# Optimization experiments

Hardware: AMD Instinct MI355X
Metric: run time of the kernel (lower is better)

The kernel has to match this reference:

```python
import jax, jax.numpy as jnp
import numpy as np

SIZE = 512
NUM_HEADS = 8
HEAD_SIZE = SIZE // NUM_HEADS
EPS = 1e-5  # GroupNorm default eps


def setup_inputs() -> dict:
    key = jax.random.key(0)
    ks = jax.random.split(key, 8)
    B, T, D = 2, 2048, SIZE
    mk = lambda k: jax.random.normal(k, (D, D), dtype=jnp.float32) / D
    return {
        "x": jax.random.normal(ks[0], (B, T, D), dtype=jnp.float32),
        "W_Q": mk(ks[1]),
        "W_K": mk(ks[2]),
        "W_V": mk(ks[3]),
        "W_G": mk(ks[4]),
        "W_O": mk(ks[5]),
        "gn_weight": jnp.ones((D,), dtype=jnp.float32),
        "gn_bias": jnp.zeros((D,), dtype=jnp.float32),
    }


def _retention(x, W_Q, W_K, W_V):
    B, T, D = x.shape
    H, dh = NUM_HEADS, HEAD_SIZE
    # projections -> (B, H, T, dh)
    q = (x @ W_Q).reshape(B, T, H, dh).transpose(0, 2, 1, 3)
    k = (x @ W_K).reshape(B, T, H, dh).transpose(0, 2, 1, 3)
    v = (x @ W_V).reshape(B, T, H, dh).transpose(0, 2, 1, 3)
    # multi-scale per-head decay: gamma_h = 1 - 2^{-5-h}
    gammas = 1.0 - jnp.exp2(-5.0 - jnp.arange(H, dtype=jnp.float32))
    idx = jnp.arange(T)
    diff = (idx[:, None] - idx[None, :]).astype(jnp.float32)  # (T, T)
    causal = diff >= 0
    # D[h, n, m] = gamma_h^{n-m} for n >= m else 0
    decay = jnp.where(causal[None], jnp.exp(diff[None] * jnp.log(gammas)[:, None, None]), 0.0)
    scores = jnp.einsum("bhtd,bhsd->bhts", q, k) / jnp.sqrt(jnp.float32(dh))
    out = jnp.einsum("bhts,bhsd->bhtd", scores * decay[None], v)
    return out.transpose(0, 2, 1, 3).reshape(B, T, D)


def _group_norm(y, weight, bias):
    # GroupNorm(NUM_HEADS, SIZE) over flattened (B*T, SIZE)
    B, T, D = y.shape
    g = y.reshape(B * T, NUM_HEADS, HEAD_SIZE)
    mean = jnp.mean(g, axis=-1, keepdims=True)
    var = jnp.var(g, axis=-1, keepdims=True)
    g = (g - mean) / jnp.sqrt(var + EPS)
    g = g.reshape(B * T, D) * weight + bias
    return g.reshape(B, T, D)


def reference(x, W_Q, W_K, W_V, W_G, W_O, gn_weight, gn_bias):
    ret = _retention(x, W_Q, W_K, W_V)          # (B, T, D)
    normed = _group_norm(ret, gn_weight, gn_bias)  # (B, T, D)
    return jax.nn.silu(x @ W_G + normed) @ W_O
```

## Files before the change

### kernel.cpp

```cpp
#include <hip/hip_runtime.h>
#include <hip/hip_bf16.h>
#include <math.h>

#define DMODEL 512
#define T_SEQ 2048
#define NH 8
#define DH 64
#define M_ROWS 4096
#define LDST 72

typedef short s16x8 __attribute__((ext_vector_type(8)));
typedef float f32x4 __attribute__((ext_vector_type(4)));

static __device__ __forceinline__ unsigned short f2bf(float f) {
  __hip_bfloat16 h = __float2bfloat16(f);
  return *(unsigned short*)&h;
}
static __device__ __forceinline__ float bf2f(unsigned short u) {
  union { unsigned int i; float f; } x; x.i = (unsigned int)u << 16; return x.f;
}
static __device__ __forceinline__ void gld16(void* lds, const void* g) {
  __builtin_amdgcn_global_load_lds(
      (const __attribute__((address_space(1))) unsigned int*)g,
      (__attribute__((address_space(3))) unsigned int*)lds, 16, 0, 0);
}

__global__ __launch_bounds__(256) void prep_k(
    const float* __restrict__ x, unsigned short* __restrict__ Xb,
    const float* __restrict__ W0, const float* __restrict__ W1,
    const float* __restrict__ W2, const float* __restrict__ W3,
    const float* __restrict__ W4, unsigned short* __restrict__ WT)
{
  __shared__ __align__(16) unsigned short buf[64 * LDST];
  const int bid = blockIdx.x, tid = threadIdx.x;
  if (bid < 1024) {
    const size_t i = ((size_t)bid * 256 + tid) * 8;
    float4 a = *(const float4*)&x[i];
    float4 b = *(const float4*)&x[i + 4];
    s16x8 o;
    o[0]=f2bf(a.x); o[1]=f2bf(a.y); o[2]=f2bf(a.z); o[3]=f2bf(a.w);
    o[4]=f2bf(b.x); o[5]=f2bf(b.y); o[6]=f2bf(b.z); o[7]=f2bf(b.w);
    *(s16x8*)&Xb[i] = o;
    return;
  }
  const int bid2 = bid - 1024;
  const int z = bid2 >> 6, rem = bid2 & 63;
  const int n0 = (rem & 7) * 64, k0 = (rem >> 3) * 64;
  const float* W = (z==0)?W0:(z==1)?W1:(z==2)?W2:(z==3)?W3:W4;
  #pragma unroll
  for (int r = 0; r < 4; ++r) {
    int idx = r * 256 + tid;
    int kr = idx >> 4, nc = idx & 15;
    float4 v = *(const float4*)&W[(size_t)(k0 + kr) * DMODEL + n0 + nc * 4];
    buf[(nc*4+0) * LDST + kr] = f2bf(v.x);
    buf[(nc*4+1) * LDST + kr] = f2bf(v.y);
    buf[(nc*4+2) * LDST + kr] = f2bf(v.z);
    buf[(nc*4+3) * LDST + kr] = f2bf(v.w);
  }
  __syncthreads();
  #pragma unroll
  for (int r = 0; r < 2; ++r) {
    int idx = r * 256 + tid;
    int nr = idx >> 3, c = idx & 7;
    *(s16x8*)&WT[((size_t)z * DMODEL + n0 + nr) * DMODEL + k0 + c * 8] =
        *(const s16x8*)&buf[nr * LDST + c * 8];
  }
}

__global__ __launch_bounds__(256) void mfma_gemm_k(
    const unsigned short* __restrict__ A, const unsigned short* __restrict__ BT,
    unsigned short* __restrict__ C0, unsigned short* __restrict__ C1,
    unsigned short* __restrict__ C2, unsigned short* __restrict__ C3)
{
  __shared__ __align__(16) unsigned short As[128 * 64];
  __shared__ __align__(16) unsigned short Bs[128 * 64];
  const int ng0 = blockIdx.x * 128;
  const int m0 = blockIdx.y * 128;
  const int z = ng0 >> 9, n0 = ng0 & 511;
  unsigned short* Cz = (z==0)?C0:(z==1)?C1:(z==2)?C2:C3;
  const int tid = threadIdx.x;
  const int wave = tid >> 6, lane = tid & 63;
  const int wm = wave >> 1, wn = wave & 1;
  const int n = lane & 15, quad = lane >> 4;

  int srow[4], scol[4];
  #pragma unroll
  for (int r = 0; r < 4; ++r) {
    int idx = r * 256 + tid;
    srow[r] = idx >> 3;
    scol[r] = ((idx & 7) ^ (srow[r] & 7)) * 8;
  }

  f32x4 acc[4][4];
  #pragma unroll
  for (int mi = 0; mi < 4; ++mi)
    #pragma unroll
    for (int ni = 0; ni < 4; ++ni) acc[mi][ni] = (f32x4){0.f,0.f,0.f,0.f};

  for (int k0 = 0; k0 < 512; k0 += 64) {
    #pragma unroll
    for (int r = 0; r < 4; ++r) {
      int idx = r * 256 + tid;
      gld16(&As[idx * 8], &A[(size_t)(m0 + srow[r]) * DMODEL + k0 + scol[r]]);
      gld16(&Bs[idx * 8], &BT[(size_t)(ng0 + srow[r]) * DMODEL + k0 + scol[r]]);
    }
    __syncthreads();
    #pragma unroll
    for (int kk = 0; kk < 2; ++kk) {
      s16x8 af[4], bf[4];
      #pragma unroll
      for (int mi = 0; mi < 4; ++mi) {
        int R = wm*64 + mi*16 + n, cc = (kk*4 + quad) ^ (n & 7);
        af[mi] = *(const s16x8*)&As[R * 64 + cc * 8];
      }
      #pragma unroll
      for (int ni = 0; ni < 4; ++ni) {
        int R = wn*64 + ni*16 + n, cc = (kk*4 + quad) ^ (n & 7);
        bf[ni] = *(const s16x8*)&Bs[R * 64 + cc * 8];
      }
      #pragma unroll
      for (int mi = 0; mi < 4; ++mi)
        #pragma unroll
        for (int ni = 0; ni < 4; ++ni)
          acc[mi][ni] = __builtin_amdgcn_mfma_f32_16x16x32_bf16(
              af[mi], bf[ni], acc[mi][ni], 0, 0, 0);
    }
    __syncthreads();
  }

  #pragma unroll
  for (int mi = 0; mi < 4; ++mi)
    #pragma unroll
    for (int ni = 0; ni < 4; ++ni)
      #pragma unroll
      for (int r = 0; r < 4; ++r)
        Cz[(size_t)(m0 + wm*64 + mi*16 + quad*4 + r) * DMODEL +
           n0 + wn*64 + ni*16 + n] = f2bf(acc[mi][ni][r]);
}

__global__ __launch_bounds__(256) void ret_kv_k(
    const unsigned short* __restrict__ Kb, const unsigned short* __restrict__ Vb,
    float* __restrict__ AT)
{
  __shared__ __align__(16) unsigned short Kts[64 * LDST];
  __shared__ __align__(16) unsigned short Vts[64 * LDST];
  const int c = blockIdx.x, h = blockIdx.y, b = blockIdx.z;
  const int bh = b * NH + h;
  const int tid = threadIdx.x;
  const int wave = tid >> 6, lane = tid & 63;
  const int n = lane & 15, quad = lane >> 4;
  const size_t base = ((size_t)b * T_SEQ + (size_t)c * 64) * DMODEL + h * DH;
  const float lg = log2f(1.0f - exp2f(-5.0f - (float)h));

  #pragma unroll
  for (int r = 0; r < 2; ++r) {
    int idx = r * 256 + tid;
    int m = idx & 63, ch = idx >> 6;
    s16x8 kv = *(const s16x8*)&Kb[base + (size_t)m * DMODEL + ch * 8];
    s16x8 vv = *(const s16x8*)&Vb[base + (size_t)m * DMODEL + ch * 8];
    float sc = exp2f((float)(64 - m) * lg);
    #pragma unroll
    for (int e = 0; e < 8; ++e) {
      Kts[(ch * 8 + e) * LDST + m] = f2bf(bf2f(((unsigned short*)&kv)[e]) * sc);
      Vts[(ch * 8 + e) * LDST + m] = ((unsigned short*)&vv)[e];
    }
  }
  __syncthreads();

  f32x4 at[4];
  #pragma unroll
  for (int j = 0; j < 4; ++j) at[j] = (f32x4){0.f,0.f,0.f,0.f};
  #pragma unroll
  for (int kk = 0; kk < 2; ++kk) {
    s16x8 a = *(const s16x8*)&Vts[(wave*16 + n) * LDST + kk*32 + quad*8];
    #pragma unroll
    for (int j = 0; j < 4; ++j) {
      s16x8 bf = *(const s16x8*)&Kts[(j*16 + n) * LDST + kk*32 + quad*8];
      at[j] = __builtin_amdgcn_mfma_f32_16x16x32_bf16(a, bf, at[j], 0, 0, 0);
    }
  }
  float* Ab = AT + (((size_t)bh * 32 + c) << 12);
  #pragma unroll
  for (int j = 0; j < 4; ++j)
    #pragma unroll
    for (int r = 0; r < 4; ++r)
      Ab[(wave*16 + quad*4 + r) * 64 + j*16 + n] = at[j][r];
}

__global__ __launch_bounds__(256) void ret_o2_k(
    const unsigned short* __restrict__ Qb, const unsigned short* __restrict__ Kb,
    const unsigned short* __restrict__ Vb, const float* __restrict__ AT,
    const unsigned short* __restrict__ Gg, const float* __restrict__ gnw,
    const float* __restrict__ gnb, unsigned short* __restrict__ Sb)
{
  __shared__ __align__(16) unsigned short Qs[64 * LDST];
  __shared__ __align__(16) unsigned short Ks[64 * LDST];
  __shared__ __align__(16) unsigned short Vst[64 * LDST];
  __shared__ __align__(16) unsigned short Ss[64 * LDST];
  __shared__ __align__(16) unsigned short Ps[64 * LDST];
  const int c = (int)gridDim.x - 1 - (int)blockIdx.x;
  const int h = blockIdx.y, b = blockIdx.z;
  const int bh = b * NH + h;
  const int tid = threadIdx.x;
  const int wave = tid >> 6, lane = tid & 63;
  const int n = lane & 15, quad = lane >> 4;
  const size_t base = ((size_t)b * T_SEQ + (size_t)c * 64) * DMODEL + h * DH;
  const float lg = log2f(1.0f - exp2f(-5.0f - (float)h));
  const float g64 = exp2f(64.0f * lg);

  #pragma unroll
  for (int r = 0; r < 2; ++r) {
    int idx = r * 256 + tid;
    int i = idx >> 3, ch = idx & 7;
    *(s16x8*)&Qs[i * LDST + ch * 8] =
        *(const s16x8*)&Qb[base + (size_t)i * DMODEL + ch * 8];
    *(s16x8*)&Ks[i * LDST + ch * 8] =
        *(const s16x8*)&Kb[base + (size_t)i * DMODEL + ch * 8];
  }
  #pragma unroll
  for (int r = 0; r < 2; ++r) {
    int idx = r * 256 + tid;
    int m = idx & 63, ch = idx >> 6;
    s16x8 vv = *(const s16x8*)&Vb[base + (size_t)m * DMODEL + ch * 8];
    #pragma unroll
    for (int e = 0; e < 8; ++e)
      Vst[(ch * 8 + e) * LDST + m] = ((unsigned short*)&vv)[e];
  }

  const float* Ac = AT + (((size_t)bh * 32) << 12) + (size_t)tid * 16;
  float4 S0 = {0,0,0,0}, S1 = S0, S2 = S0, S3 = S0;
  if (c > 0) {
    float4 n0 = *(const float4*)(Ac + 0);
    float4 n1 = *(const float4*)(Ac + 4);
    float4 n2 = *(const float4*)(Ac + 8);
    float4 n3 = *(const float4*)(Ac + 12);
    for (int cp = 0; cp < c; ++cp) {
      float4 a0 = n0, a1 = n1, a2 = n2, a3 = n3;
      if (cp + 1 < c) {
        const float* p = Ac + ((size_t)(cp + 1) << 12);
        n0 = *(const float4*)(p + 0);  n1 = *(const float4*)(p + 4);
        n2 = *(const float4*)(p + 8);  n3 = *(const float4*)(p + 12);
      }
      S0.x = fmaf(g64, S0.x, a0.x); S0.y = fmaf(g64, S0.y, a0.y);
      S0.z = fmaf(g64, S0.z, a0.z); S0.w = fmaf(g64, S0.w, a0.w);
      S1.x = fmaf(g64, S1.x, a1.x); S1.y = fmaf(g64, S1.y, a1.y);
      S1.z = fmaf(g64, S1.z, a1.z); S1.w = fmaf(g64, S1.w, a1.w);
      S2.x = fmaf(g64, S2.x, a2.x); S2.y = fmaf(g64, S2.y, a2.y);
      S2.z = fmaf(g64, S2.z, a2.z); S2.w = fmaf(g64, S2.w, a2.w);
      S3.x = fmaf(g64, S3.x, a3.x); S3.y = fmaf(g64, S3.y, a3.y);
      S3.z = fmaf(g64, S3.z, a3.z); S3.w = fmaf(g64, S3.w, a3.w);
    }
  }
  {
    const int d2 = tid >> 2, d1b = (tid & 3) * 16;
    s16x8 lo, hi;
    lo[0]=f2bf(S0.x); lo[1]=f2bf(S0.y); lo[2]=f2bf(S0.z); lo[3]=f2bf(S0.w);
    lo[4]=f2bf(S1.x); lo[5]=f2bf(S1.y); lo[6]=f2bf(S1.z); lo[7]=f2bf(S1.w);
    hi[0]=f2bf(S2.x); hi[1]=f2bf(S2.y); hi[2]=f2bf(S2.z); hi[3]=f2bf(S2.w);
    hi[4]=f2bf(S3.x); hi[5]=f2bf(S3.y); hi[6]=f2bf(S3.z); hi[7]=f2bf(S3.w);
    *(s16x8*)&Ss[d2 * LDST + d1b] = lo;
    *(s16x8*)&Ss[d2 * LDST + d1b + 8] = hi;
  }
  __syncthreads();

  f32x4 s[4], u[4];
  #pragma unroll
  for (int j = 0; j < 4; ++j) {
    s[j] = (f32x4){0.f,0.f,0.f,0.f};
    u[j] = (f32x4){0.f,0.f,0.f,0.f};
  }
  #pragma unroll
  for (int kk = 0; kk < 2; ++kk) {
    s16x8 a = *(const s16x8*)&Qs[(wave*16 + n) * LDST + kk*32 + quad*8];
    #pragma unroll
    for (int j = 0; j < 4; ++j) {
      s16x8 bk = *(const s16x8*)&Ks[(j*16 + n) * LDST + kk*32 + quad*8];
      s[j] = __builtin_amdgcn_mfma_f32_16x16x32_bf16(a, bk, s[j], 0, 0, 0);
      s16x8 bs = *(const s16x8*)&Ss[(j*16 + n) * LDST + kk*32 + quad*8];
      u[j] = __builtin_amdgcn_mfma_f32_16x16x32_bf16(a, bs, u[j], 0, 0, 0);
    }
  }

  float rowf[4], colf[4];
  #pragma unroll
  for (int r = 0; r < 4; ++r) rowf[r] = exp2f((float)(wave*16 + quad*4 + r) * lg);
  #pragma unroll
  for (int j = 0; j < 4; ++j) colf[j] = exp2f(-(float)(j*16 + n) * lg);

  #pragma unroll
  for (int j = 0; j < 4; ++j)
    #pragma unroll
    for (int r = 0; r < 4; ++r) {
      int i = wave*16 + quad*4 + r, mcol = j*16 + n;
      float v = (mcol <= i) ? s[j][r] * 0.125f * rowf[r] * colf[j] : 0.0f;
      Ps[i * LDST + mcol] = f2bf(v);
    }
  __syncthreads();

  f32x4 acc[4];
  #pragma unroll
  for (int j = 0; j < 4; ++j) acc[j] = (f32x4){0.f,0.f,0.f,0.f};
  #pragma unroll
  for (int kk = 0; kk < 2; ++kk) {
    s16x8 a = *(const s16x8*)&Ps[(wave*16 + n) * LDST + kk*32 + quad*8];
    #pragma unroll
    for (int j = 0; j < 4; ++j) {
      s16x8 bf = *(const s16x8*)&Vst[(j*16 + n) * LDST + kk*32 + quad*8];
      acc[j] = __builtin_amdgcn_mfma_f32_16x16x32_bf16(a, bf, acc[j], 0, 0, 0);
    }
  }

  float ov[4][4];
  #pragma unroll
  for (int j = 0; j < 4; ++j)
    #pragma unroll
    for (int r = 0; r < 4; ++r)
      ov[j][r] = acc[j][r] + 0.125f * rowf[r] * u[j][r];

  float gw[4], gb[4];
  #pragma unroll
  for (int j = 0; j < 4; ++j) {
    gw[j] = gnw[h*DH + j*16 + n];
    gb[j] = gnb[h*DH + j*16 + n];
  }

  #pragma unroll
  for (int r = 0; r < 4; ++r) {
    float sum = ov[0][r] + ov[1][r] + ov[2][r] + ov[3][r];
    float sq  = ov[0][r]*ov[0][r] + ov[1][r]*ov[1][r]
              + ov[2][r]*ov[2][r] + ov[3][r]*ov[3][r];
    #pragma unroll
    for (int off = 8; off > 0; off >>= 1) {
      sum += __shfl_xor(sum, off, 64);
      sq  += __shfl_xor(sq,  off, 64);
    }
    const float mean = sum * (1.0f / 64.0f);
    float var = sq * (1.0f / 64.0f) - mean * mean;
    var = fmaxf(var, 0.0f);
    const float rstd = rsqrtf(var + 1e-5f);
    const int i = wave*16 + quad*4 + r;
    const size_t rowoff = base + (size_t)i * DMODEL;
    #pragma unroll
    for (int j = 0; j < 4; ++j) {
      float normed = (ov[j][r] - mean) * rstd * gw[j] + gb[j];
      float uu = bf2f(Gg[rowoff + j*16 + n]) + normed;
      Sb[rowoff + j*16 + n] = f2bf(uu / (1.0f + expf(-uu)));
    }
  }
}

__global__ __launch_bounds__(256) void out_gemm_k(
    const unsigned short* __restrict__ A, const unsigned short* __restrict__ BT,
    float* __restrict__ out)
{
  __shared__ __align__(16) unsigned short As[128 * 64];
  __shared__ __align__(16) unsigned short Bs[128 * 64];
  const int n0 = blockIdx.x * 128;
  const int m0 = blockIdx.y * 128;
  const int tid = threadIdx.x;
  const int wave = tid >> 6, lane = tid & 63;
  const int wm = wave >> 1, wn = wave & 1;
  const int n = lane & 15, quad = lane >> 4;

  int srow[4], scol[4];
  #pragma unroll
  for (int r = 0; r < 4; ++r) {
    int idx = r * 256 + tid;
    srow[r] = idx >> 3;
    scol[r] = ((idx & 7) ^ (srow[r] & 7)) * 8;
  }

  f32x4 acc[4][4];
  #pragma unroll
  for (int mi = 0; mi < 4; ++mi)
    #pragma unroll
    for (int ni = 0; ni < 4; ++ni) acc[mi][ni] = (f32x4){0.f,0.f,0.f,0.f};

  for (int k0 = 0; k0 < 512; k0 += 64) {
    #pragma unroll
    for (int r = 0; r < 4; ++r) {
      int idx = r * 256 + tid;
      gld16(&As[idx * 8], &A[(size_t)(m0 + srow[r]) * DMODEL + k0 + scol[r]]);
      gld16(&Bs[idx * 8], &BT[(size_t)(n0 + srow[r]) * DMODEL + k0 + scol[r]]);
    }
    __syncthreads();
    #pragma unroll
    for (int kk = 0; kk < 2; ++kk) {
      s16x8 af[4], bf[4];
      #pragma unroll
      for (int mi = 0; mi < 4; ++mi) {
        int R = wm*64 + mi*16 + n, cc = (kk*4 + quad) ^ (n & 7);
        af[mi] = *(const s16x8*)&As[R * 64 + cc * 8];
      }
      #pragma unroll
      for (int ni = 0; ni < 4; ++ni) {
        int R = wn*64 + ni*16 + n, cc = (kk*4 + quad) ^ (n & 7);
        bf[ni] = *(const s16x8*)&Bs[R * 64 + cc * 8];
      }
      #pragma unroll
      for (int mi = 0; mi < 4; ++mi)
        #pragma unroll
        for (int ni = 0; ni < 4; ++ni)
          acc[mi][ni] = __builtin_amdgcn_mfma_f32_16x16x32_bf16(
              af[mi], bf[ni], acc[mi][ni], 0, 0, 0);
    }
    __syncthreads();
  }

  #pragma unroll
  for (int mi = 0; mi < 4; ++mi)
    #pragma unroll
    for (int ni = 0; ni < 4; ++ni)
      #pragma unroll
      for (int r = 0; r < 4; ++r)
        out[(size_t)(m0 + wm*64 + mi*16 + quad*4 + r) * DMODEL +
            n0 + wn*64 + ni*16 + n] = acc[mi][ni][r];
}

extern "C" void kernel_launch(void* const* d_in, const int* in_sizes, int n_in,
                              void* d_out, int out_size, void* d_ws, size_t ws_size,
                              hipStream_t stream) {
  const float* x   = (const float*)d_in[0];
  const float* WQ  = (const float*)d_in[1];
  const float* WK  = (const float*)d_in[2];
  const float* WV  = (const float*)d_in[3];
  const float* WG  = (const float*)d_in[4];
  const float* WO  = (const float*)d_in[5];
  const float* gnw = (const float*)d_in[6];
  const float* gnb = (const float*)d_in[7];
  float* out = (float*)d_out;

  char* ws = (char*)d_ws;
  unsigned short* Xb = (unsigned short*)(ws);
  unsigned short* Qb = (unsigned short*)(ws + 4  * (1<<20));
  unsigned short* Kb = (unsigned short*)(ws + 8  * (1<<20));
  unsigned short* Vb = (unsigned short*)(ws + 12 * (1<<20));
  unsigned short* G  = (unsigned short*)(ws + 16 * (1<<20));
  float* AT  = (float*)(ws + 24 * (1<<20));
  unsigned short* Sb = (unsigned short*)(ws + 32 * (1<<20));
  unsigned short* WT = (unsigned short*)(ws + 40 * (1<<20));
  (void)ws_size;

  prep_k<<<dim3(1024 + 320), 256, 0, stream>>>(x, Xb, WQ, WK, WV, WG, WO, WT);
  mfma_gemm_k<<<dim3(16, M_ROWS / 128), 256, 0, stream>>>(
      Xb, WT, Qb, Kb, Vb, G);
  ret_kv_k<<<dim3(T_SEQ / 64, NH, 2), 256, 0, stream>>>(Kb, Vb, AT);
  ret_o2_k<<<dim3(T_SEQ / 64, NH, 2), 256, 0, stream>>>(
      Qb, Kb, Vb, AT, G, gnw, gnb, Sb);
  out_gemm_k<<<dim3(4, M_ROWS / 128), 256, 0, stream>>>(
      Sb, WT + 4 * DMODEL * DMODEL, out);
}
```

Measured before the change: 130.0 us.

## Fuse chunk KV-state computation into projection GEMM epilogue; shrink output GEMM tile

Result: faster. 125.5 us (-3.4%).

```diff
diff --git a/kernel.cpp b/kernel.cpp
--- a/kernel.cpp
+++ b/kernel.cpp
@@ -47,6 +47,12 @@
   const int z = bid2 >> 6, rem = bid2 & 63;
   const int n0 = (rem & 7) * 64, k0 = (rem >> 3) * 64;
   const float* W = (z==0)?W0:(z==1)?W1:(z==2)?W2:(z==3)?W3:W4;
+  int rowbase;
+  if (z == 0)      rowbase = n0;
+  else if (z == 1) rowbase = 512 + (n0 >> 6) * 128;
+  else if (z == 2) rowbase = 512 + (n0 >> 6) * 128 + 64;
+  else if (z == 3) rowbase = 1536 + n0;
+  else             rowbase = 2048 + n0;
   #pragma unroll
   for (int r = 0; r < 4; ++r) {
     int idx = r * 256 + tid;
@@ -62,22 +68,22 @@
   for (int r = 0; r < 2; ++r) {
     int idx = r * 256 + tid;
     int nr = idx >> 3, c = idx & 7;
-    *(s16x8*)&WT[((size_t)z * DMODEL + n0 + nr) * DMODEL + k0 + c * 8] =
+    *(s16x8*)&WT[((size_t)(rowbase + nr)) * DMODEL + k0 + c * 8] =
         *(const s16x8*)&buf[nr * LDST + c * 8];
   }
 }
 
-__global__ __launch_bounds__(256) void mfma_gemm_k(
+__global__ __launch_bounds__(256) void proj_kv_k(
     const unsigned short* __restrict__ A, const unsigned short* __restrict__ BT,
-    unsigned short* __restrict__ C0, unsigned short* __restrict__ C1,
-    unsigned short* __restrict__ C2, unsigned short* __restrict__ C3)
+    unsigned short* __restrict__ Qb, unsigned short* __restrict__ Kb,
+    unsigned short* __restrict__ Vb, unsigned short* __restrict__ Gb,
+    float* __restrict__ AT)
 {
-  __shared__ __align__(16) unsigned short As[128 * 64];
-  __shared__ __align__(16) unsigned short Bs[128 * 64];
+  __shared__ __align__(16) unsigned short smem[2 * 128 * 64];
+  unsigned short* As = smem;
+  unsigned short* Bs = smem + 128 * 64;
   const int ng0 = blockIdx.x * 128;
   const int m0 = blockIdx.y * 128;
-  const int z = ng0 >> 9, n0 = ng0 & 511;
-  unsigned short* Cz = (z==0)?C0:(z==1)?C1:(z==2)?C2:C3;
   const int tid = threadIdx.x;
   const int wave = tid >> 6, lane = tid & 63;
   const int wm = wave >> 1, wn = wave & 1;
@@ -128,63 +134,73 @@
     __syncthreads();
   }
 
+  const int bx = blockIdx.x;
+  if (bx < 4 || bx >= 12) {
+    unsigned short* Cz = (bx < 4) ? Qb : Gb;
+    const int n0 = (bx < 4) ? ng0 : (ng0 - 1536);
+    #pragma unroll
+    for (int mi = 0; mi < 4; ++mi)
+      #pragma unroll
+      for (int ni = 0; ni < 4; ++ni)
+        #pragma unroll
+        for (int r = 0; r < 4; ++r)
+          Cz[(size_t)(m0 + wm*64 + mi*16 + quad*4 + r) * DMODEL +
+             n0 + wn*64 + ni*16 + n] = f2bf(acc[mi][ni][r]);
+    return;
+  }
+
+  const int h = (ng0 - 512) >> 7;
+  const float lg = log2f(1.0f - exp2f(-5.0f - (float)h));
+  unsigned short* KVo = (wn == 0) ? Kb : Vb;
   #pragma unroll
   for (int mi = 0; mi < 4; ++mi)
     #pragma unroll
     for (int ni = 0; ni < 4; ++ni)
       #pragma unroll
       for (int r = 0; r < 4; ++r)
-        Cz[(size_t)(m0 + wm*64 + mi*16 + quad*4 + r) * DMODEL +
-           n0 + wn*64 + ni*16 + n] = f2bf(acc[mi][ni][r]);
-}
-
-__global__ __launch_bounds__(256) void ret_kv_k(
-    const unsigned short* __restrict__ Kb, const unsigned short* __restrict__ Vb,
-    float* __restrict__ AT)
-{
-  __shared__ __align__(16) unsigned short Kts[64 * LDST];
-  __shared__ __align__(16) unsigned short Vts[64 * LDST];
-  const int c = blockIdx.x, h = blockIdx.y, b = blockIdx.z;
-  const int bh = b * NH + h;
-  const int tid = threadIdx.x;
-  const int wave = tid >> 6, lane = tid & 63;
-  const int n = lane & 15, quad = lane >> 4;
-  const size_t base = ((size_t)b * T_SEQ + (size_t)c * 64) * DMODEL + h * DH;
-  const float lg = log2f(1.0f - exp2f(-5.0f - (float)h));
-
-  #pragma unroll
-  for (int r = 0; r < 2; ++r) {
-    int idx = r * 256 + tid;
-    int m = idx & 63, ch = idx >> 6;
-    s16x8 kv = *(const s16x8*)&Kb[base + (size_t)m * DMODEL + ch * 8];
-    s16x8 vv = *(const s16x8*)&Vb[base + (size_t)m * DMODEL + ch * 8];
-    float sc = exp2f((float)(64 - m) * lg);
-    #pragma unroll
-    for (int e = 0; e < 8; ++e) {
-      Kts[(ch * 8 + e) * LDST + m] = f2bf(bf2f(((unsigned short*)&kv)[e]) * sc);
-      Vts[(ch * 8 + e) * LDST + m] = ((unsigned short*)&vv)[e];
-    }
-  }
-  __syncthreads();
-
-  f32x4 at[4];
-  #pragma unroll
-  for (int j = 0; j < 4; ++j) at[j] = (f32x4){0.f,0.f,0.f,0.f};
-  #pragma unroll
-  for (int kk = 0; kk < 2; ++kk) {
-    s16x8 a = *(const s16x8*)&Vts[(wave*16 + n) * LDST + kk*32 + quad*8];
-    #pragma unroll
-    for (int j = 0; j < 4; ++j) {
-      s16x8 bf = *(const s16x8*)&Kts[(j*16 + n) * LDST + kk*32 + quad*8];
-      at[j] = __builtin_amdgcn_mfma_f32_16x16x32_bf16(a, bf, at[j], 0, 0, 0);
-    }
-  }
-  float* Ab = AT + (((size_t)bh * 32 + c) << 12);
-  #pragma unroll
-  for (int j = 0; j < 4; ++j)
-    #pragma unroll
-    for (int r = 0; r < 4; ++r)
-      Ab[(wave*16 + quad*4 + r) * 64 + j*16 + n] = at[j][r];
+        KVo[(size_t)(m0 + wm*64 + mi*16 + quad*4 + r) * DMODEL +
+            h*DH + ni*16 + n] = f2bf(acc[mi][ni][r]);
+
+  unsigned short* Kt = smem;
+  unsigned short* Vt = smem + 64 * LDST;
+  #pragma unroll
+  for (int cc2 = 0; cc2 < 2; ++cc2) {
+    __syncthreads();
+    if (wm == cc2) {
+      unsigned short* Tt = (wn == 0) ? Kt : Vt;
+      #pragma unroll
+      for (int mi = 0; mi < 4; ++mi)
+        #pragma unroll
+        for (int r = 0; r < 4; ++r) {
+          int m = mi*16 + quad*4 + r;
+          float sc = (wn == 0) ? exp2f((float)(64 - m) * lg) : 1.0f;
+          #pragma unroll
+          for (int ni = 0; ni < 4; ++ni)
+            Tt[(ni*16 + n) * LDST + m] = f2bf(acc[mi][ni][r] * sc);
+        }
+    }
+    __syncthreads();
+    f32x4 at[4];
+    #pragma unroll
+    for (int j = 0; j < 4; ++j) at[j] = (f32x4){0.f,0.f,0.f,0.f};
+    #pragma unroll
+    for (int kk = 0; kk < 2; ++kk) {
+      s16x8 a = *(const s16x8*)&Vt[(wave*16 + n) * LDST + kk*32 + quad*8];
+      #pragma unroll
+      for (int j = 0; j < 4; ++j) {
+        s16x8 bf = *(const s16x8*)&Kt[(j*16 + n) * LDST + kk*32 + quad*8];
+        at[j] = __builtin_amdgcn_mfma_f32_16x16x32_bf16(a, bf, at[j], 0, 0, 0);
+      }
+    }
+    const int gr = m0 + cc2 * 64;
+    const int bb = gr >> 11, cchunk = (gr & 2047) >> 6;
+    float* Ab = AT + (((size_t)(bb * NH + h) * 32 + cchunk) << 12);
+    #pragma unroll
+    for (int j = 0; j < 4; ++j)
+      #pragma unroll
+      for (int r = 0; r < 4; ++r)
+        Ab[(wave*16 + quad*4 + r) * 64 + j*16 + n] = at[j][r];
+  }
 }
 
 __global__ __launch_bounds__(256) void ret_o2_k(
@@ -338,8 +354,7 @@
     float var = sq * (1.0f / 64.0f) - mean * mean;
     var = fmaxf(var, 0.0f);
     const float rstd = rsqrtf(var + 1e-5f);
-    const int i = wave*16 + quad*4 + r;
-    const size_t rowoff = base + (size_t)i * DMODEL;
+    const size_t rowoff = base + (size_t)(wave*16 + quad*4 + r) * DMODEL;
     #pragma unroll
     for (int j = 0; j < 4; ++j) {
       float normed = (ov[j][r] - mean) * rstd * gw[j] + gb[j];
@@ -354,8 +369,8 @@
     float* __restrict__ out)
 {
   __shared__ __align__(16) unsigned short As[128 * 64];
-  __shared__ __align__(16) unsigned short Bs[128 * 64];
-  const int n0 = blockIdx.x * 128;
+  __shared__ __align__(16) unsigned short Bs[64 * 64];
+  const int n0 = blockIdx.x * 64;
   const int m0 = blockIdx.y * 128;
   const int tid = threadIdx.x;
   const int wave = tid >> 6, lane = tid & 63;
@@ -370,37 +385,41 @@
     scol[r] = ((idx & 7) ^ (srow[r] & 7)) * 8;
   }
 
-  f32x4 acc[4][4];
+  f32x4 acc[4][2];
   #pragma unroll
   for (int mi = 0; mi < 4; ++mi)
     #pragma unroll
-    for (int ni = 0; ni < 4; ++ni) acc[mi][ni] = (f32x4){0.f,0.f,0.f,0.f};
+    for (int ni = 0; ni < 2; ++ni) acc[mi][ni] = (f32x4){0.f,0.f,0.f,0.f};
 
   for (int k0 = 0; k0 < 512; k0 += 64) {
     #pragma unroll
     for (int r = 0; r < 4; ++r) {
       int idx = r * 256 + tid;
       gld16(&As[idx * 8], &A[(size_t)(m0 + srow[r]) * DMODEL + k0 + scol[r]]);
+    }
+    #pragma unroll
+    for (int r = 0; r < 2; ++r) {
+      int idx = r * 256 + tid;
       gld16(&Bs[idx * 8], &BT[(size_t)(n0 + srow[r]) * DMODEL + k0 + scol[r]]);
     }
     __syncthreads();
     #pragma unroll
     for (int kk = 0; kk < 2; ++kk) {
-      s16x8 af[4], bf[4];
+      s16x8 af[4], bf[2];
       #pragma unroll
       for (int mi = 0; mi < 4; ++mi) {
         int R = wm*64 + mi*16 + n, cc = (kk*4 + quad) ^ (n & 7);
         af[mi] = *(const s16x8*)&As[R * 64 + cc * 8];
       }
       #pragma unroll
-      for (int ni = 0; ni < 4; ++ni) {
-        int R = wn*64 + ni*16 + n, cc = (kk*4 + quad) ^ (n & 7);
+      for (int ni = 0; ni < 2; ++ni) {
+        int R = wn*32 + ni*16 + n, cc = (kk*4 + quad) ^ (n & 7);
         bf[ni] = *(const s16x8*)&Bs[R * 64 + cc * 8];
       }
       #pragma unroll
       for (int mi = 0; mi < 4; ++mi)
         #pragma unroll
-        for (int ni = 0; ni < 4; ++ni)
+        for (int ni = 0; ni < 2; ++ni)
           acc[mi][ni] = __builtin_amdgcn_mfma_f32_16x16x32_bf16(
               af[mi], bf[ni], acc[mi][ni], 0, 0, 0);
     }
@@ -410,11 +429,11 @@
   #pragma unroll
   for (int mi = 0; mi < 4; ++mi)
     #pragma unroll
-    for (int ni = 0; ni < 4; ++ni)
+    for (int ni = 0; ni < 2; ++ni)
       #pragma unroll
       for (int r = 0; r < 4; ++r)
         out[(size_t)(m0 + wm*64 + mi*16 + quad*4 + r) * DMODEL +
-            n0 + wn*64 + ni*16 + n] = acc[mi][ni][r];
+            n0 + wn*32 + ni*16 + n] = acc[mi][ni][r];
 }
 
 extern "C" void kernel_launch(void* const* d_in, const int* in_sizes, int n_in,
@@ -442,11 +461,10 @@
   (void)ws_size;
 
   prep_k<<<dim3(1024 + 320), 256, 0, stream>>>(x, Xb, WQ, WK, WV, WG, WO, WT);
-  mfma_gemm_k<<<dim3(16, M_ROWS / 128), 256, 0, stream>>>(
-      Xb, WT, Qb, Kb, Vb, G);
-  ret_kv_k<<<dim3(T_SEQ / 64, NH, 2), 256, 0, stream>>>(Kb, Vb, AT);
+  proj_kv_k<<<dim3(16, M_ROWS / 128), 256, 0, stream>>>(
+      Xb, WT, Qb, Kb, Vb, G, AT);
   ret_o2_k<<<dim3(T_SEQ / 64, NH, 2), 256, 0, stream>>>(
       Qb, Kb, Vb, AT, G, gnw, gnb, Sb);
-  out_gemm_k<<<dim3(4, M_ROWS / 128), 256, 0, stream>>>(
-      Sb, WT + 4 * DMODEL * DMODEL, out);
-}
+  out_gemm_k<<<dim3(8, M_ROWS / 128), 256, 0, stream>>>(
+      Sb, WT + 2048 * DMODEL, out);
+}
```
